# Kernel optimization log

Hardware: AMD Instinct MI355X
Metric: run time of the kernel (lower is better)

## Reference

```python
import jax, jax.numpy as jnp
import numpy as np

B, N = 2, 2000
C_IN, RH, RW = 256, 7, 7
D_FLAT = C_IN * RH * RW  # 12544
D_OUT = 1024
NUM_CLASSES = 10


def setup_inputs() -> dict:
    key = jax.random.key(0)
    ks = jax.random.split(key, 10)
    s1 = 1.0 / np.sqrt(D_FLAT)
    s2 = 1.0 / np.sqrt(D_OUT)
    return {
        "features": jax.random.normal(ks[0], (B, N, C_IN, RH, RW), jnp.float32),
        "boxes": jax.random.normal(ks[1], (B, N, 5), jnp.float32),
        "w1": jax.random.uniform(ks[2], (D_FLAT, D_OUT), jnp.float32, -s1, s1),
        "b1": jax.random.uniform(ks[3], (D_OUT,), jnp.float32, -s1, s1),
        "w2": jax.random.uniform(ks[4], (D_OUT, D_OUT), jnp.float32, -s2, s2),
        "b2": jax.random.uniform(ks[5], (D_OUT,), jnp.float32, -s2, s2),
        "wc": jax.random.uniform(ks[6], (D_OUT, NUM_CLASSES + 1), jnp.float32, -s2, s2),
        "bc": jax.random.uniform(ks[7], (NUM_CLASSES + 1,), jnp.float32, -s2, s2),
        "wr": jax.random.uniform(ks[8], (D_OUT, 5), jnp.float32, -s2, s2),
        "br": jax.random.uniform(ks[9], (5,), jnp.float32, -s2, s2),
    }


def reference(features, boxes, w1, b1, w2, b2, wc, bc, wr, br):
    # Flatten(start_dim=2): [B, N, C*7*7]
    x = features.reshape(B, N, D_FLAT)
    # fc: Linear -> ReLU -> Linear -> ReLU
    h = jax.nn.relu(jnp.einsum("bnd,de->bne", x, w1) + b1)
    h = jax.nn.relu(jnp.einsum("bnd,de->bne", h, w2) + b2)
    classification = jnp.einsum("bnd,dc->bnc", h, wc) + bc  # [B, N, num_classes+1]
    regression = jnp.einsum("bnd,dr->bnr", h, wr) + br      # [B, N, 5]
    boxes_out = boxes + regression
    rois = boxes
    return classification, boxes_out, rois
```

## Files before the change

kernel.cpp:

```cpp
#include <hip/hip_runtime.h>
#include <stdint.h>

#define GAS __attribute__((address_space(1)))
#define LAS __attribute__((address_space(3)))

typedef short bf16x8 __attribute__((ext_vector_type(8)));
typedef float f32x4 __attribute__((ext_vector_type(4)));
typedef unsigned short u16x8 __attribute__((ext_vector_type(8)));

__device__ __forceinline__ unsigned short f2bf(float f) {
  union { float f; uint32_t u; } v; v.f = f;
  uint32_t r = v.u + 0x7FFFu + ((v.u >> 16) & 1u);
  return (unsigned short)(r >> 16);
}

__global__ __launch_bounds__(256) void cvt_kernel(const float* __restrict__ src,
                                                  unsigned short* __restrict__ dst,
                                                  long n8) {
  long i = (long)blockIdx.x * blockDim.x + threadIdx.x;
  if (i >= n8) return;
  const float4* s4 = (const float4*)src;
  float4 a = s4[i * 2];
  float4 b = s4[i * 2 + 1];
  u16x8 o;
  o[0] = f2bf(a.x); o[1] = f2bf(a.y); o[2] = f2bf(a.z); o[3] = f2bf(a.w);
  o[4] = f2bf(b.x); o[5] = f2bf(b.y); o[6] = f2bf(b.z); o[7] = f2bf(b.w);
  ((u16x8*)dst)[i] = o;
}

__global__ __launch_bounds__(256) void transpose_cvt(const float* __restrict__ src,
                                                     unsigned short* __restrict__ dst,
                                                     int R, int C) {
  __shared__ unsigned short tile[32][33];
  int tx = threadIdx.x, ty = threadIdx.y;
  int r0 = blockIdx.y * 32, c0 = blockIdx.x * 32;
#pragma unroll
  for (int i = 0; i < 32; i += 8)
    tile[ty + i][tx] = f2bf(src[(long)(r0 + ty + i) * C + c0 + tx]);
  __syncthreads();
#pragma unroll
  for (int i = 0; i < 32; i += 8)
    dst[(long)(c0 + ty + i) * R + r0 + tx] = tile[tx][ty + i];
}

__global__ __launch_bounds__(256) void bias_relu_cvt(const float* __restrict__ acc,
                                                     const float* __restrict__ bias,
                                                     unsigned short* __restrict__ dst) {
  long i = (long)blockIdx.x * 256 + threadIdx.x;
  const float4* a4 = (const float4*)acc;
  float4 a = a4[i * 2];
  float4 b = a4[i * 2 + 1];
  int col = (int)((i * 8) & 1023);
  const float4* b4 = (const float4*)(bias + col);
  float4 ba = b4[0], bb = b4[1];
  u16x8 o;
  o[0] = f2bf(fmaxf(a.x + ba.x, 0.f)); o[1] = f2bf(fmaxf(a.y + ba.y, 0.f));
  o[2] = f2bf(fmaxf(a.z + ba.z, 0.f)); o[3] = f2bf(fmaxf(a.w + ba.w, 0.f));
  o[4] = f2bf(fmaxf(b.x + bb.x, 0.f)); o[5] = f2bf(fmaxf(b.y + bb.y, 0.f));
  o[6] = f2bf(fmaxf(b.z + bb.z, 0.f)); o[7] = f2bf(fmaxf(b.w + bb.w, 0.f));
  ((u16x8*)dst)[i] = o;
}

__global__ __launch_bounds__(256, 2) void gemm1_atomic(const unsigned short* __restrict__ A,
                                                       const unsigned short* __restrict__ Bt,
                                                       float* __restrict__ Cv, int M, int K,
                                                       int kIters) {
  __shared__ unsigned short lA[128 * 64];
  __shared__ unsigned short lB[128 * 64];
  const int tid = threadIdx.x;
  const int lane = tid & 63;
  const int wave = tid >> 6;
  const int wm = wave >> 1, wn = wave & 1;

  const int b = blockIdx.x;
  const int xcd = b & 7;
  const int slot = b >> 3;
  const int bx = slot & 7;
  const int pg = xcd * 16 + (slot >> 3);
  const int by = pg & 31;
  const int bz = pg >> 5;

  const long rowBase = (long)by * 128;
  const long colBase = (long)bx * 128;
  const int kStart = bz * kIters * 64;

  f32x4 acc[4][4];
#pragma unroll
  for (int i = 0; i < 4; i++)
#pragma unroll
    for (int j = 0; j < 4; j++) acc[i][j] = (f32x4){0.f, 0.f, 0.f, 0.f};

  long gA[4], gB[4];
#pragma unroll
  for (int it = 0; it < 4; ++it) {
    int f = it * 256 + tid;
    int r = f >> 3;
    int q = f & 7;
    int kq = ((q ^ (r & 7)) * 8) + kStart;
    long ar = rowBase + r;
    if (ar >= M) ar = M - 1;
    gA[it] = ar * (long)K + kq;
    gB[it] = ((long)(colBase + r)) * K + kq;
  }

  for (int ki = 0; ki < kIters; ++ki) {
    const long kc = (long)ki * 64;
#pragma unroll
    for (int it = 0; it < 4; ++it) {
      int f = it * 256 + tid;
      __builtin_amdgcn_global_load_lds((const GAS void*)(A + gA[it] + kc),
                                       (LAS void*)(lA + f * 8), 16, 0, 0);
    }
#pragma unroll
    for (int it = 0; it < 4; ++it) {
      int f = it * 256 + tid;
      __builtin_amdgcn_global_load_lds((const GAS void*)(Bt + gB[it] + kc),
                                       (LAS void*)(lB + f * 8), 16, 0, 0);
    }
    __syncthreads();
#pragma unroll
    for (int ks = 0; ks < 64; ks += 32) {
      bf16x8 af[4], bf[4];
      const int c = (ks >> 3) + (lane >> 4);
      const int slotk = (c ^ (lane & 7)) << 3;
      const int mr = wm * 64 + (lane & 15);
      const int nr = wn * 64 + (lane & 15);
#pragma unroll
      for (int i = 0; i < 4; i++)
        af[i] = *(const bf16x8*)(lA + (mr + i * 16) * 64 + slotk);
#pragma unroll
      for (int i = 0; i < 4; i++)
        bf[i] = *(const bf16x8*)(lB + (nr + i * 16) * 64 + slotk);
#pragma unroll
      for (int i = 0; i < 4; i++)
#pragma unroll
        for (int j = 0; j < 4; j++)
          acc[i][j] = __builtin_amdgcn_mfma_f32_16x16x32_bf16(af[i], bf[j], acc[i][j], 0, 0, 0);
    }
    __syncthreads();
  }

  const int cq = lane & 15;
  const int rq = (lane >> 4) * 4;
#pragma unroll
  for (int i = 0; i < 4; i++) {
#pragma unroll
    for (int j = 0; j < 4; j++) {
      int col = (int)colBase + wn * 64 + j * 16 + cq;
#pragma unroll
      for (int r = 0; r < 4; r++) {
        long grow = rowBase + wm * 64 + i * 16 + rq + r;
        if (grow < M) unsafeAtomicAdd(&Cv[grow * 1024 + col], acc[i][j][r]);
      }
    }
  }
}

__global__ __launch_bounds__(256, 2) void gemm2_direct(const unsigned short* __restrict__ A,
                                                       const unsigned short* __restrict__ Bt,
                                                       const float* __restrict__ bias,
                                                       float* __restrict__ Cv, int M) {
  const int K = 1024;
  __shared__ unsigned short lA[128 * 64];
  __shared__ unsigned short lB[64 * 64];
  const int tid = threadIdx.x;
  const int lane = tid & 63;
  const int wave = tid >> 6;
  const int wm = wave >> 1, wn = wave & 1;

  const int b = blockIdx.x;
  const int xcd = b & 7;
  const int slot = b >> 3;
  const int bx = slot & 15;
  const int by = xcd * 4 + (slot >> 4);

  const long rowBase = (long)by * 128;
  const long colBase = (long)bx * 64;

  f32x4 acc[4][2];
#pragma unroll
  for (int i = 0; i < 4; i++)
#pragma unroll
    for (int j = 0; j < 2; j++) acc[i][j] = (f32x4){0.f, 0.f, 0.f, 0.f};

  long gA[4], gB[2];
#pragma unroll
  for (int it = 0; it < 4; ++it) {
    int f = it * 256 + tid;
    int r = f >> 3;
    int q = f & 7;
    int kq = (q ^ (r & 7)) * 8;
    long ar = rowBase + r;
    if (ar >= M) ar = M - 1;
    gA[it] = ar * (long)K + kq;
  }
#pragma unroll
  for (int it = 0; it < 2; ++it) {
    int f = it * 256 + tid;
    int r = f >> 3;
    int q = f & 7;
    int kq = (q ^ (r & 7)) * 8;
    gB[it] = ((long)(colBase + r)) * K + kq;
  }

  for (int ki = 0; ki < 16; ++ki) {
    const long kc = (long)ki * 64;
#pragma unroll
    for (int it = 0; it < 4; ++it) {
      int f = it * 256 + tid;
      __builtin_amdgcn_global_load_lds((const GAS void*)(A + gA[it] + kc),
                                       (LAS void*)(lA + f * 8), 16, 0, 0);
    }
#pragma unroll
    for (int it = 0; it < 2; ++it) {
      int f = it * 256 + tid;
      __builtin_amdgcn_global_load_lds((const GAS void*)(Bt + gB[it] + kc),
                                       (LAS void*)(lB + f * 8), 16, 0, 0);
    }
    __syncthreads();
#pragma unroll
    for (int ks = 0; ks < 64; ks += 32) {
      bf16x8 af[4], bf[2];
      const int c = (ks >> 3) + (lane >> 4);
      const int slotk = (c ^ (lane & 7)) << 3;
      const int mr = wm * 64 + (lane & 15);
      const int nr = wn * 32 + (lane & 15);
#pragma unroll
      for (int i = 0; i < 4; i++)
        af[i] = *(const bf16x8*)(lA + (mr + i * 16) * 64 + slotk);
#pragma unroll
      for (int j = 0; j < 2; j++)
        bf[j] = *(const bf16x8*)(lB + (nr + j * 16) * 64 + slotk);
#pragma unroll
      for (int i = 0; i < 4; i++)
#pragma unroll
        for (int j = 0; j < 2; j++)
          acc[i][j] = __builtin_amdgcn_mfma_f32_16x16x32_bf16(af[i], bf[j], acc[i][j], 0, 0, 0);
    }
    __syncthreads();
  }

  const int cq = lane & 15;
  const int rq = (lane >> 4) * 4;
#pragma unroll
  for (int i = 0; i < 4; i++) {
#pragma unroll
    for (int j = 0; j < 2; j++) {
      int col = (int)colBase + wn * 32 + j * 16 + cq;
      float bv = bias[col];
#pragma unroll
      for (int r = 0; r < 4; r++) {
        long grow = rowBase + wm * 64 + i * 16 + rq + r;
        if (grow < M) {
          float v = acc[i][j][r] + bv;
          Cv[grow * 1024 + col] = v > 0.f ? v : 0.f;
        }
      }
    }
  }
}

__global__ __launch_bounds__(256) void head_kernel(
    const float* __restrict__ H2, const float* __restrict__ wc, const float* __restrict__ bc,
    const float* __restrict__ wr, const float* __restrict__ br, const float* __restrict__ boxes,
    float* __restrict__ cls, float* __restrict__ bout, float* __restrict__ rois) {
  const int lane = threadIdx.x & 63;
  const int wave = threadIdx.x >> 6;
  const int row = blockIdx.x * 4 + wave;
  const float* h = H2 + (long)row * 1024;
  float acc[16];
#pragma unroll
  for (int c = 0; c < 16; c++) acc[c] = 0.f;
#pragma unroll
  for (int i = 0; i < 16; i++) {
    int d = i * 64 + lane;
    float hv = h[d];
#pragma unroll
    for (int c = 0; c < 11; c++) acc[c] += hv * wc[d * 11 + c];
#pragma unroll
    for (int c = 0; c < 5; c++) acc[11 + c] += hv * wr[d * 5 + c];
  }
#pragma unroll
  for (int off = 32; off >= 1; off >>= 1) {
#pragma unroll
    for (int c = 0; c < 16; c++) acc[c] += __shfl_down(acc[c], off);
  }
  if (lane == 0) {
#pragma unroll
    for (int c = 0; c < 11; c++) cls[row * 11 + c] = acc[c] + bc[c];
#pragma unroll
    for (int c = 0; c < 5; c++) {
      float rg = acc[11 + c] + br[c];
      float bx = boxes[row * 5 + c];
      bout[row * 5 + c] = bx + rg;
      rois[row * 5 + c] = bx;
    }
  }
}

extern "C" void kernel_launch(void* const* d_in, const int* in_sizes, int n_in,
                              void* d_out, int out_size, void* d_ws, size_t ws_size,
                              hipStream_t stream) {
  const float* features = (const float*)d_in[0];
  const float* boxes = (const float*)d_in[1];
  const float* w1 = (const float*)d_in[2];
  const float* b1 = (const float*)d_in[3];
  const float* w2 = (const float*)d_in[4];
  const float* b2 = (const float*)d_in[5];
  const float* wc = (const float*)d_in[6];
  const float* bc = (const float*)d_in[7];
  const float* wr = (const float*)d_in[8];
  const float* br = (const float*)d_in[9];

  char* ws = (char*)d_ws;
  unsigned short* Xb  = (unsigned short*)ws;
  unsigned short* W1T = (unsigned short*)(ws + 100352000);
  unsigned short* W2T = (unsigned short*)(ws + 126042112);
  unsigned short* H1  = (unsigned short*)(ws + 128139264);
  float*          H1f = (float*)(ws + 136331264);
  float*          H2  = (float*)(ws + 152715264);

  hipMemsetAsync(H1f, 0, 16384000, stream);
  cvt_kernel<<<24500, 256, 0, stream>>>(features, Xb, 6272000);
  transpose_cvt<<<dim3(32, 392), dim3(32, 8), 0, stream>>>(w1, W1T, 12544, 1024);
  transpose_cvt<<<dim3(32, 32), dim3(32, 8), 0, stream>>>(w2, W2T, 1024, 1024);
  gemm1_atomic<<<1024, 256, 0, stream>>>(Xb, W1T, H1f, 4000, 12544, 49);
  bias_relu_cvt<<<2000, 256, 0, stream>>>(H1f, b1, H1);
  gemm2_direct<<<512, 256, 0, stream>>>(H1, W2T, b2, H2, 4000);
  float* cls = (float*)d_out;
  float* bout = cls + 44000;
  float* rois = cls + 64000;
  head_kernel<<<1000, 256, 0, stream>>>(H2, wc, bc, wr, br, boxes, cls, bout, rois);
}
```

Measured before the change: 529.3 us.

## Rewrite GEMM1 as 8-wave 256x256 tile kernel with double-buffered LDS prefetch

The first large GEMM moves from a 4-wave 128x128 tile with a single LDS buffer to an 8-wave 256x256 tile. It double-buffers 128KB of LDS so global-to-LDS loads for the next K step are issued while MFMAs run on the current buffer. It also splits the work into four phases with barriers and setprio to interleave loads and math. The grid drops to 256 blocks, and the split-K factor of 4 with atomic accumulation is kept. The costs are a single block per CU because of the LDS size, higher register pressure from 128 accumulator floats, and fewer blocks to cover tail imbalance.

```diff
diff --git a/kernel.cpp b/kernel.cpp
--- a/kernel.cpp
+++ b/kernel.cpp
@@ -61,95 +61,135 @@
   ((u16x8*)dst)[i] = o;
 }
 
-__global__ __launch_bounds__(256, 2) void gemm1_atomic(const unsigned short* __restrict__ A,
-                                                       const unsigned short* __restrict__ Bt,
-                                                       float* __restrict__ Cv, int M, int K,
-                                                       int kIters) {
-  __shared__ unsigned short lA[128 * 64];
-  __shared__ unsigned short lB[128 * 64];
+__global__ __launch_bounds__(512, 2) void gemm1_8w(const unsigned short* __restrict__ A,
+                                                   const unsigned short* __restrict__ Bt,
+                                                   float* __restrict__ Cv, int M, int K,
+                                                   int kIters) {
+  __shared__ unsigned short lds[65536];
   const int tid = threadIdx.x;
   const int lane = tid & 63;
   const int wave = tid >> 6;
-  const int wm = wave >> 1, wn = wave & 1;
+  const int wm = wave >> 2;
+  const int wn = wave & 3;
 
   const int b = blockIdx.x;
   const int xcd = b & 7;
   const int slot = b >> 3;
-  const int bx = slot & 7;
-  const int pg = xcd * 16 + (slot >> 3);
-  const int by = pg & 31;
-  const int bz = pg >> 5;
-
-  const long rowBase = (long)by * 128;
-  const long colBase = (long)bx * 128;
+  const int panel = xcd + 8 * (slot >> 4);
+  const int bz = panel >> 2;
+  const int bx = panel & 3;
+  const int by = slot & 15;
+
+  const long rowBase = (long)by * 256;
+  const long colBase = (long)bx * 256;
   const int kStart = bz * kIters * 64;
 
-  f32x4 acc[4][4];
-#pragma unroll
-  for (int i = 0; i < 4; i++)
+  f32x4 acc[8][4];
+#pragma unroll
+  for (int i = 0; i < 8; i++)
 #pragma unroll
     for (int j = 0; j < 4; j++) acc[i][j] = (f32x4){0.f, 0.f, 0.f, 0.f};
 
-  long gA[4], gB[4];
-#pragma unroll
-  for (int it = 0; it < 4; ++it) {
-    int f = it * 256 + tid;
-    int r = f >> 3;
-    int q = f & 7;
+  long g8[8];
+  int ldsOff8[8];
+#pragma unroll
+  for (int i = 0; i < 8; ++i) {
+    int flat = i * 512 + tid;
+    int s = flat & 2047;
+    int r = s >> 3;
+    int q = s & 7;
     int kq = ((q ^ (r & 7)) * 8) + kStart;
-    long ar = rowBase + r;
-    if (ar >= M) ar = M - 1;
-    gA[it] = ar * (long)K + kq;
-    gB[it] = ((long)(colBase + r)) * K + kq;
-  }
-
-  for (int ki = 0; ki < kIters; ++ki) {
-    const long kc = (long)ki * 64;
-#pragma unroll
-    for (int it = 0; it < 4; ++it) {
-      int f = it * 256 + tid;
-      __builtin_amdgcn_global_load_lds((const GAS void*)(A + gA[it] + kc),
-                                       (LAS void*)(lA + f * 8), 16, 0, 0);
-    }
-#pragma unroll
-    for (int it = 0; it < 4; ++it) {
-      int f = it * 256 + tid;
-      __builtin_amdgcn_global_load_lds((const GAS void*)(Bt + gB[it] + kc),
-                                       (LAS void*)(lB + f * 8), 16, 0, 0);
-    }
-    __syncthreads();
-#pragma unroll
-    for (int ks = 0; ks < 64; ks += 32) {
-      bf16x8 af[4], bf[4];
-      const int c = (ks >> 3) + (lane >> 4);
-      const int slotk = (c ^ (lane & 7)) << 3;
-      const int mr = wm * 64 + (lane & 15);
-      const int nr = wn * 64 + (lane & 15);
-#pragma unroll
-      for (int i = 0; i < 4; i++)
-        af[i] = *(const bf16x8*)(lA + (mr + i * 16) * 64 + slotk);
-#pragma unroll
-      for (int i = 0; i < 4; i++)
-        bf[i] = *(const bf16x8*)(lB + (nr + i * 16) * 64 + slotk);
-#pragma unroll
-      for (int i = 0; i < 4; i++)
-#pragma unroll
-        for (int j = 0; j < 4; j++)
-          acc[i][j] = __builtin_amdgcn_mfma_f32_16x16x32_bf16(af[i], bf[j], acc[i][j], 0, 0, 0);
-    }
-    __syncthreads();
+    long row;
+    if (flat >= 2048) {
+      row = colBase + r;
+    } else {
+      row = rowBase + r;
+      if (row >= M) row = M - 1;
+    }
+    g8[i] = row * (long)K + kq;
+    ldsOff8[i] = flat * 8;
+  }
+
+#pragma unroll
+  for (int i = 0; i < 8; ++i) {
+    const unsigned short* src = (i < 4) ? A : Bt;
+    __builtin_amdgcn_global_load_lds((const GAS void*)(src + g8[i]),
+                                     (LAS void*)(lds + ldsOff8[i]), 16, 0, 0);
+  }
+  asm volatile("s_waitcnt vmcnt(0)" ::: "memory");
+  __builtin_amdgcn_s_barrier();
+  asm volatile("" ::: "memory");
+
+  const int l15 = lane & 15;
+  const int lxor = lane & 7;
+  const int chi = lane >> 4;
+
+  for (int t = 0; t < kIters; ++t) {
+    const int cb = (t & 1) << 15;
+    const int nb = cb ^ 32768;
+    const long kc = (long)(t + 1) * 64;
+    const bool doStage = (t + 1 < kIters);
+
+#pragma unroll
+    for (int p = 0; p < 4; ++p) {
+      const int qi = p >> 1;
+      const int qj = p & 1;
+      bf16x8 af[4][2], bf[2][2];
+#pragma unroll
+      for (int ks = 0; ks < 2; ++ks) {
+        const int slotk = (((ks * 4 + chi) ^ lxor) << 3);
+#pragma unroll
+        for (int i = 0; i < 4; ++i) {
+          const int mr = wm * 128 + qi * 64 + i * 16 + l15;
+          af[i][ks] = *(const bf16x8*)(lds + cb + mr * 64 + slotk);
+        }
+#pragma unroll
+        for (int j = 0; j < 2; ++j) {
+          const int nr = wn * 64 + qj * 32 + j * 16 + l15;
+          bf[j][ks] = *(const bf16x8*)(lds + cb + 16384 + nr * 64 + slotk);
+        }
+      }
+      if (doStage && p < 2) {
+#pragma unroll
+        for (int l = 0; l < 4; ++l) {
+          const int idx = p * 4 + l;
+          const unsigned short* src = (idx < 4) ? A : Bt;
+          __builtin_amdgcn_global_load_lds((const GAS void*)(src + g8[idx] + kc),
+                                           (LAS void*)(lds + nb + ldsOff8[idx]), 16, 0, 0);
+        }
+      }
+      __builtin_amdgcn_s_barrier();
+      asm volatile("s_waitcnt lgkmcnt(0)" ::: "memory");
+      __builtin_amdgcn_sched_barrier(0);
+      __builtin_amdgcn_s_setprio(1);
+#pragma unroll
+      for (int i = 0; i < 4; ++i)
+#pragma unroll
+        for (int j = 0; j < 2; ++j) {
+          acc[qi * 4 + i][qj * 2 + j] = __builtin_amdgcn_mfma_f32_16x16x32_bf16(
+              af[i][0], bf[j][0], acc[qi * 4 + i][qj * 2 + j], 0, 0, 0);
+          acc[qi * 4 + i][qj * 2 + j] = __builtin_amdgcn_mfma_f32_16x16x32_bf16(
+              af[i][1], bf[j][1], acc[qi * 4 + i][qj * 2 + j], 0, 0, 0);
+        }
+      __builtin_amdgcn_s_setprio(0);
+      if (p == 3) {
+        asm volatile("s_waitcnt vmcnt(0)" ::: "memory");
+      }
+      __builtin_amdgcn_s_barrier();
+    }
+    asm volatile("" ::: "memory");
   }
 
   const int cq = lane & 15;
-  const int rq = (lane >> 4) * 4;
-#pragma unroll
-  for (int i = 0; i < 4; i++) {
-#pragma unroll
-    for (int j = 0; j < 4; j++) {
-      int col = (int)colBase + wn * 64 + j * 16 + cq;
-#pragma unroll
-      for (int r = 0; r < 4; r++) {
-        long grow = rowBase + wm * 64 + i * 16 + rq + r;
+  const int rq = (lane >> 4) << 2;
+#pragma unroll
+  for (int i = 0; i < 8; ++i) {
+#pragma unroll
+    for (int j = 0; j < 4; ++j) {
+      const int col = (int)colBase + wn * 64 + j * 16 + cq;
+#pragma unroll
+      for (int r = 0; r < 4; ++r) {
+        long grow = rowBase + wm * 128 + i * 16 + rq + r;
         if (grow < M) unsafeAtomicAdd(&Cv[grow * 1024 + col], acc[i][j][r]);
       }
     }
@@ -324,7 +364,7 @@
   cvt_kernel<<<24500, 256, 0, stream>>>(features, Xb, 6272000);
   transpose_cvt<<<dim3(32, 392), dim3(32, 8), 0, stream>>>(w1, W1T, 12544, 1024);
   transpose_cvt<<<dim3(32, 32), dim3(32, 8), 0, stream>>>(w2, W2T, 1024, 1024);
-  gemm1_atomic<<<1024, 256, 0, stream>>>(Xb, W1T, H1f, 4000, 12544, 49);
+  gemm1_8w<<<256, 512, 0, stream>>>(Xb, W1T, H1f, 4000, 12544, 49);
   bias_relu_cvt<<<2000, 256, 0, stream>>>(H1f, b1, H1);
   gemm2_direct<<<512, 256, 0, stream>>>(H1, W2T, b2, H2, 4000);
   float* cls = (float*)d_out;
```

After: 532.2 us. Within noise of the previous version (+0.6%).

## Fuse fp32-to-bf16 conversion into GEMM A-loads and bias-ReLU into GEMM2

Applied to the files above, without the earlier changes.

GEMM1 now reads fp32 features directly and converts them to bf16 while staging into LDS, which removes the separate conversion pass and its bf16 workspace round trip. GEMM2 likewise reads the fp32 atomic accumulator, adds bias1, applies ReLU and converts to bf16 during the A-tile load, so the bias_relu_cvt kernel goes away. The two weight transposes are merged into one launch. The cost is that the A loads become register-staged fp32 loads instead of async global-to-LDS copies, which doubles A-side load bytes inside the GEMMs and may stall the MFMA loop because nothing is pipelined.

```diff
diff --git a/kernel.cpp b/kernel.cpp
--- a/kernel.cpp
+++ b/kernel.cpp
@@ -14,26 +14,22 @@
   return (unsigned short)(r >> 16);
 }
 
-__global__ __launch_bounds__(256) void cvt_kernel(const float* __restrict__ src,
-                                                  unsigned short* __restrict__ dst,
-                                                  long n8) {
-  long i = (long)blockIdx.x * blockDim.x + threadIdx.x;
-  if (i >= n8) return;
-  const float4* s4 = (const float4*)src;
-  float4 a = s4[i * 2];
-  float4 b = s4[i * 2 + 1];
-  u16x8 o;
-  o[0] = f2bf(a.x); o[1] = f2bf(a.y); o[2] = f2bf(a.z); o[3] = f2bf(a.w);
-  o[4] = f2bf(b.x); o[5] = f2bf(b.y); o[6] = f2bf(b.z); o[7] = f2bf(b.w);
-  ((u16x8*)dst)[i] = o;
-}
-
-__global__ __launch_bounds__(256) void transpose_cvt(const float* __restrict__ src,
-                                                     unsigned short* __restrict__ dst,
-                                                     int R, int C) {
+__global__ __launch_bounds__(256) void prep_transpose(const float* __restrict__ w1,
+                                                      const float* __restrict__ w2,
+                                                      unsigned short* __restrict__ W1T,
+                                                      unsigned short* __restrict__ W2T) {
   __shared__ unsigned short tile[32][33];
   int tx = threadIdx.x, ty = threadIdx.y;
-  int r0 = blockIdx.y * 32, c0 = blockIdx.x * 32;
+  const float* src;
+  unsigned short* dst;
+  int R, yb;
+  if ((int)blockIdx.y < 392) {
+    src = w1; dst = W1T; R = 12544; yb = blockIdx.y;
+  } else {
+    src = w2; dst = W2T; R = 1024; yb = blockIdx.y - 392;
+  }
+  const int C = 1024;
+  int r0 = yb * 32, c0 = blockIdx.x * 32;
 #pragma unroll
   for (int i = 0; i < 32; i += 8)
     tile[ty + i][tx] = f2bf(src[(long)(r0 + ty + i) * C + c0 + tx]);
@@ -43,28 +39,10 @@
     dst[(long)(c0 + ty + i) * R + r0 + tx] = tile[tx][ty + i];
 }
 
-__global__ __launch_bounds__(256) void bias_relu_cvt(const float* __restrict__ acc,
-                                                     const float* __restrict__ bias,
-                                                     unsigned short* __restrict__ dst) {
-  long i = (long)blockIdx.x * 256 + threadIdx.x;
-  const float4* a4 = (const float4*)acc;
-  float4 a = a4[i * 2];
-  float4 b = a4[i * 2 + 1];
-  int col = (int)((i * 8) & 1023);
-  const float4* b4 = (const float4*)(bias + col);
-  float4 ba = b4[0], bb = b4[1];
-  u16x8 o;
-  o[0] = f2bf(fmaxf(a.x + ba.x, 0.f)); o[1] = f2bf(fmaxf(a.y + ba.y, 0.f));
-  o[2] = f2bf(fmaxf(a.z + ba.z, 0.f)); o[3] = f2bf(fmaxf(a.w + ba.w, 0.f));
-  o[4] = f2bf(fmaxf(b.x + bb.x, 0.f)); o[5] = f2bf(fmaxf(b.y + bb.y, 0.f));
-  o[6] = f2bf(fmaxf(b.z + bb.z, 0.f)); o[7] = f2bf(fmaxf(b.w + bb.w, 0.f));
-  ((u16x8*)dst)[i] = o;
-}
-
-__global__ __launch_bounds__(256, 2) void gemm1_atomic(const unsigned short* __restrict__ A,
-                                                       const unsigned short* __restrict__ Bt,
-                                                       float* __restrict__ Cv, int M, int K,
-                                                       int kIters) {
+__global__ __launch_bounds__(256, 2) void gemm1_f32a(const float* __restrict__ A,
+                                                     const unsigned short* __restrict__ Bt,
+                                                     float* __restrict__ Cv, int M, int K,
+                                                     int kIters) {
   __shared__ unsigned short lA[128 * 64];
   __shared__ unsigned short lB[128 * 64];
   const int tid = threadIdx.x;
@@ -91,6 +69,7 @@
     for (int j = 0; j < 4; j++) acc[i][j] = (f32x4){0.f, 0.f, 0.f, 0.f};
 
   long gA[4], gB[4];
+  int aLds[4];
 #pragma unroll
   for (int it = 0; it < 4; ++it) {
     int f = it * 256 + tid;
@@ -101,21 +80,25 @@
     if (ar >= M) ar = M - 1;
     gA[it] = ar * (long)K + kq;
     gB[it] = ((long)(colBase + r)) * K + kq;
+    aLds[it] = f * 8;
   }
 
   for (int ki = 0; ki < kIters; ++ki) {
     const long kc = (long)ki * 64;
-#pragma unroll
-    for (int it = 0; it < 4; ++it) {
-      int f = it * 256 + tid;
-      __builtin_amdgcn_global_load_lds((const GAS void*)(A + gA[it] + kc),
-                                       (LAS void*)(lA + f * 8), 16, 0, 0);
-    }
 #pragma unroll
     for (int it = 0; it < 4; ++it) {
       int f = it * 256 + tid;
       __builtin_amdgcn_global_load_lds((const GAS void*)(Bt + gB[it] + kc),
                                        (LAS void*)(lB + f * 8), 16, 0, 0);
+    }
+#pragma unroll
+    for (int it = 0; it < 4; ++it) {
+      const float4* p = (const float4*)(A + gA[it] + kc);
+      float4 a = p[0], c = p[1];
+      u16x8 v;
+      v[0] = f2bf(a.x); v[1] = f2bf(a.y); v[2] = f2bf(a.z); v[3] = f2bf(a.w);
+      v[4] = f2bf(c.x); v[5] = f2bf(c.y); v[6] = f2bf(c.z); v[7] = f2bf(c.w);
+      *(u16x8*)(lA + aLds[it]) = v;
     }
     __syncthreads();
 #pragma unroll
@@ -156,10 +139,11 @@
   }
 }
 
-__global__ __launch_bounds__(256, 2) void gemm2_direct(const unsigned short* __restrict__ A,
-                                                       const unsigned short* __restrict__ Bt,
-                                                       const float* __restrict__ bias,
-                                                       float* __restrict__ Cv, int M) {
+__global__ __launch_bounds__(256, 2) void gemm2_fused(const float* __restrict__ H1f,
+                                                      const float* __restrict__ bias1,
+                                                      const unsigned short* __restrict__ Bt,
+                                                      const float* __restrict__ bias2,
+                                                      float* __restrict__ Cv, int M) {
   const int K = 1024;
   __shared__ unsigned short lA[128 * 64];
   __shared__ unsigned short lB[64 * 64];
@@ -183,7 +167,8 @@
 #pragma unroll
     for (int j = 0; j < 2; j++) acc[i][j] = (f32x4){0.f, 0.f, 0.f, 0.f};
 
-  long gA[4], gB[2];
+  long gA[4];
+  int aLds[4], aKq[4];
 #pragma unroll
   for (int it = 0; it < 4; ++it) {
     int f = it * 256 + tid;
@@ -193,7 +178,10 @@
     long ar = rowBase + r;
     if (ar >= M) ar = M - 1;
     gA[it] = ar * (long)K + kq;
-  }
+    aLds[it] = f * 8;
+    aKq[it] = kq;
+  }
+  long gB[2];
 #pragma unroll
   for (int it = 0; it < 2; ++it) {
     int f = it * 256 + tid;
@@ -206,16 +194,23 @@
   for (int ki = 0; ki < 16; ++ki) {
     const long kc = (long)ki * 64;
 #pragma unroll
-    for (int it = 0; it < 4; ++it) {
-      int f = it * 256 + tid;
-      __builtin_amdgcn_global_load_lds((const GAS void*)(A + gA[it] + kc),
-                                       (LAS void*)(lA + f * 8), 16, 0, 0);
-    }
-#pragma unroll
     for (int it = 0; it < 2; ++it) {
       int f = it * 256 + tid;
       __builtin_amdgcn_global_load_lds((const GAS void*)(Bt + gB[it] + kc),
                                        (LAS void*)(lB + f * 8), 16, 0, 0);
+    }
+#pragma unroll
+    for (int it = 0; it < 4; ++it) {
+      const float4* p = (const float4*)(H1f + gA[it] + kc);
+      const float4* bp = (const float4*)(bias1 + kc + aKq[it]);
+      float4 a = p[0], c = p[1];
+      float4 ba = bp[0], bb = bp[1];
+      u16x8 v;
+      v[0] = f2bf(fmaxf(a.x + ba.x, 0.f)); v[1] = f2bf(fmaxf(a.y + ba.y, 0.f));
+      v[2] = f2bf(fmaxf(a.z + ba.z, 0.f)); v[3] = f2bf(fmaxf(a.w + ba.w, 0.f));
+      v[4] = f2bf(fmaxf(c.x + bb.x, 0.f)); v[5] = f2bf(fmaxf(c.y + bb.y, 0.f));
+      v[6] = f2bf(fmaxf(c.z + bb.z, 0.f)); v[7] = f2bf(fmaxf(c.w + bb.w, 0.f));
+      *(u16x8*)(lA + aLds[it]) = v;
     }
     __syncthreads();
 #pragma unroll
@@ -247,7 +242,7 @@
 #pragma unroll
     for (int j = 0; j < 2; j++) {
       int col = (int)colBase + wn * 32 + j * 16 + cq;
-      float bv = bias[col];
+      float bv = bias2[col];
 #pragma unroll
       for (int r = 0; r < 4; r++) {
         long grow = rowBase + wm * 64 + i * 16 + rq + r;
@@ -313,20 +308,15 @@
   const float* br = (const float*)d_in[9];
 
   char* ws = (char*)d_ws;
-  unsigned short* Xb  = (unsigned short*)ws;
-  unsigned short* W1T = (unsigned short*)(ws + 100352000);
-  unsigned short* W2T = (unsigned short*)(ws + 126042112);
-  unsigned short* H1  = (unsigned short*)(ws + 128139264);
-  float*          H1f = (float*)(ws + 136331264);
-  float*          H2  = (float*)(ws + 152715264);
+  unsigned short* W1T = (unsigned short*)ws;
+  unsigned short* W2T = (unsigned short*)(ws + 25690112);
+  float*          H1f = (float*)(ws + 27787264);
+  float*          H2  = (float*)(ws + 44171264);
 
   hipMemsetAsync(H1f, 0, 16384000, stream);
-  cvt_kernel<<<24500, 256, 0, stream>>>(features, Xb, 6272000);
-  transpose_cvt<<<dim3(32, 392), dim3(32, 8), 0, stream>>>(w1, W1T, 12544, 1024);
-  transpose_cvt<<<dim3(32, 32), dim3(32, 8), 0, stream>>>(w2, W2T, 1024, 1024);
-  gemm1_atomic<<<1024, 256, 0, stream>>>(Xb, W1T, H1f, 4000, 12544, 49);
-  bias_relu_cvt<<<2000, 256, 0, stream>>>(H1f, b1, H1);
-  gemm2_direct<<<512, 256, 0, stream>>>(H1, W2T, b2, H2, 4000);
+  prep_transpose<<<dim3(32, 424), dim3(32, 8), 0, stream>>>(w1, w2, W1T, W2T);
+  gemm1_f32a<<<1024, 256, 0, stream>>>(features, W1T, H1f, 4000, 12544, 49);
+  gemm2_fused<<<512, 256, 0, stream>>>(H1f, b1, W2T, b2, H2, 4000);
   float* cls = (float*)d_out;
   float* bout = cls + 44000;
   float* rois = cls + 64000;
```

Measured after the change: 550.4 us. 1.04x slower.
